# Kernel optimization log

Hardware: AMD Instinct MI355X
Metric: run time of the kernel (lower is better)

Reference implementation:

```python
import jax, jax.numpy as jnp
import numpy as np

NUM_HEADS = 16

def setup_inputs() -> dict:
    key = jax.random.key(0)
    k1, k2, k3 = jax.random.split(key, 3)
    B, S, D = 4, 2048, 1024
    x = jax.random.normal(k1, (B, S, D), dtype=jnp.float32)
    w_qkv = jax.random.normal(k2, (D, 3 * D), dtype=jnp.float32) * (1.0 / np.sqrt(D))
    b_qkv = jnp.zeros((3 * D,), dtype=jnp.float32)
    w_out = jax.random.normal(k3, (D, D), dtype=jnp.float32) * (1.0 / np.sqrt(D))
    b_out = jnp.zeros((D,), dtype=jnp.float32)
    return {"x": x, "w_qkv": w_qkv, "b_qkv": b_qkv, "w_out": w_out, "b_out": b_out}

def reference(x, w_qkv, b_qkv, w_out, b_out):
    B, S, D = x.shape
    H = NUM_HEADS
    Dh = D // H
    # fused QKV projection: [B,S,3D]
    qkv = jnp.einsum('bsd,de->bse', x, w_qkv) + b_qkv
    q, k, v = jnp.split(qkv, 3, axis=-1)
    # separate heads -> [B,H,S,Dh]
    def heads(t):
        return t.reshape(B, S, H, Dh).transpose(0, 2, 1, 3)
    q, k, v = heads(q), heads(k), heads(v)
    # scaled dot-product attention (no mask, no dropout)
    scale = 1.0 / jnp.sqrt(jnp.asarray(Dh, dtype=x.dtype))
    attn = jnp.einsum('bhqd,bhkd->bhqk', q, k) * scale
    weights = jax.nn.softmax(attn, axis=-1)
    out = jnp.einsum('bhqk,bhkd->bhqd', weights, v)
    # combine heads -> [B,S,D], then output projection
    out = out.transpose(0, 2, 1, 3).reshape(B, S, D)
    return jnp.einsum('bsd,de->bse', out, w_out) + b_out
```

## Files before the change

### kernel.cpp

```cpp
#include <hip/hip_runtime.h>

typedef unsigned short u16;
typedef __attribute__((ext_vector_type(8))) short v8s;
typedef __attribute__((ext_vector_type(4))) float v4f;

#define MFMA16(a, b, c) __builtin_amdgcn_mfma_f32_16x16x32_bf16(a, b, c, 0, 0, 0)

static __device__ __forceinline__ u16 f32_to_bf16(float f) {
    unsigned int u = __builtin_bit_cast(unsigned int, f);
    u += 0x7fffu + ((u >> 16) & 1u);
    return (u16)(u >> 16);
}
static __device__ __forceinline__ v8s cvt8(v4f lo, v4f hi) {
    v8s r;
#pragma unroll
    for (int i = 0; i < 4; i++) {
        r[i]     = (short)f32_to_bf16(lo[i]);
        r[i + 4] = (short)f32_to_bf16(hi[i]);
    }
    return r;
}
static __device__ __forceinline__ void gload16(const void* g, void* l) {
    __builtin_amdgcn_global_load_lds(
        (const __attribute__((address_space(1))) unsigned int*)g,
        (__attribute__((address_space(3))) unsigned int*)l, 16, 0, 0);
}

__global__ void transpose_f32_bf16(const float* __restrict__ in,
                                   u16* __restrict__ out, int R, int C) {
    __shared__ u16 t[32][33];
    const int tid = threadIdx.x;
    const int tx = tid & 31, ty = tid >> 5;
    const int c0 = blockIdx.x * 32, r0 = blockIdx.y * 32;
#pragma unroll
    for (int i = 0; i < 32; i += 8)
        t[ty + i][tx] = f32_to_bf16(in[(size_t)(r0 + ty + i) * C + c0 + tx]);
    __syncthreads();
#pragma unroll
    for (int i = 0; i < 32; i += 8)
        out[(size_t)(c0 + ty + i) * R + r0 + tx] = t[tx][ty + i];
}

template <int AMODE, int CMODE>
__global__ __launch_bounds__(256)
void gemm_bt(const void* __restrict__ A, int lda,
             const u16* __restrict__ Bt, int ldb,
             const float* __restrict__ bias,
             void* __restrict__ Cq, u16* __restrict__ Kb, u16* __restrict__ VtG,
             int ldc, int K) {
    constexpr int LDA_T = AMODE ? 48 : 32;
    __shared__ __align__(16) u16 As[128 * LDA_T];
    __shared__ __align__(16) u16 Bs[128 * 32];

    const int tid  = threadIdx.x;
    const int wid  = tid >> 6;
    const int lane = tid & 63;
    const int l15  = lane & 15;
    const int quad = lane >> 4;
    const int bm = blockIdx.y * 128;
    const int bn = blockIdx.x * 128;
    const int wm = (wid & 1) * 64;
    const int wn = (wid >> 1) * 64;

    const int drow = wid * 16 + (lane >> 2);
    const int dcol = (lane & 3) * 8;
    const int ar = tid >> 2;
    const int ag = (tid & 3) * 8;

    const float* Af = (const float*)A;
    const u16*   Au = (const u16*)A;

    v4f acc[4][4];
#pragma unroll
    for (int i = 0; i < 4; i++)
#pragma unroll
        for (int j = 0; j < 4; j++) acc[i][j] = (v4f)0.f;

    for (int kb = 0; kb < K; kb += 32) {
        v8s a0, a1;
        if (AMODE) {
            const float* p0 = Af + (size_t)(bm + ar) * lda + kb + ag;
            const float* p1 = Af + (size_t)(bm + 64 + ar) * lda + kb + ag;
            v4f x00 = *(const v4f*)p0, x01 = *(const v4f*)(p0 + 4);
            v4f x10 = *(const v4f*)p1, x11 = *(const v4f*)(p1 + 4);
            a0 = cvt8(x00, x01);
            a1 = cvt8(x10, x11);
        }
        __syncthreads();
        if (AMODE) {
            *(v8s*)&As[ar * 48 + ag]        = a0;
            *(v8s*)&As[(ar + 64) * 48 + ag] = a1;
        } else {
            gload16(Au + (size_t)(bm + drow) * lda + kb + dcol,
                    &As[drow * 32 + dcol]);
            gload16(Au + (size_t)(bm + 64 + drow) * lda + kb + dcol,
                    &As[(drow + 64) * 32 + dcol]);
        }
        gload16(Bt + (size_t)(bn + drow) * ldb + kb + dcol,
                &Bs[drow * 32 + dcol]);
        gload16(Bt + (size_t)(bn + 64 + drow) * ldb + kb + dcol,
                &Bs[(drow + 64) * 32 + dcol]);
        __syncthreads();

        v8s af[4], bf[4];
#pragma unroll
        for (int mt = 0; mt < 4; mt++)
            af[mt] = *(const v8s*)&As[(wm + mt * 16 + l15) * LDA_T + quad * 8];
#pragma unroll
        for (int nt = 0; nt < 4; nt++)
            bf[nt] = *(const v8s*)&Bs[(wn + nt * 16 + l15) * 32 + quad * 8];
#pragma unroll
        for (int mt = 0; mt < 4; mt++)
#pragma unroll
            for (int nt = 0; nt < 4; nt++)
                acc[mt][nt] = MFMA16(af[mt], bf[nt], acc[mt][nt]);
    }

#pragma unroll
    for (int nt = 0; nt < 4; nt++) {
        const int n = bn + wn + nt * 16 + l15;
        const float bv = bias[n];
#pragma unroll
        for (int mt = 0; mt < 4; mt++) {
#pragma unroll
            for (int r = 0; r < 4; r++) {
                const int m = bm + wm + mt * 16 + quad * 4 + r;
                const float val = acc[mt][nt][r] + bv;
                if (CMODE == 1) {
                    ((float*)Cq)[(size_t)m * ldc + n] = val;
                } else {
                    const u16 o = f32_to_bf16(val);
                    const int region = n >> 10, nl = n & 1023;
                    if (region == 0) {
                        ((u16*)Cq)[(size_t)m * 1024 + nl] = o;
                    } else if (region == 1) {
                        Kb[(size_t)m * 1024 + nl] = o;
                    } else {
                        const int h = nl >> 6, dh = nl & 63;
                        const int b = m >> 11, s = m & 2047;
                        VtG[((size_t)((b * 16 + h) * 64 + dh)) * 2048 + s] = o;
                    }
                }
            }
        }
    }
}

__global__ __launch_bounds__(256)
void attn_fused(u16* __restrict__ Qb, const u16* __restrict__ Kb,
                const u16* __restrict__ VtG) {
    __shared__ __align__(16) u16 Ks[64 * 72];
    __shared__ __align__(16) u16 Vs[64 * 72];
    __shared__ __align__(16) u16 Ps[4 * 16 * 72];

    const int tid  = threadIdx.x;
    const int wid  = tid >> 6;
    const int lane = tid & 63;
    const int l15  = lane & 15;
    const int quad = lane >> 4;
    const int qt = blockIdx.x;
    const int h  = blockIdx.y;
    const int bz = blockIdx.z;

    const size_t qbase = (size_t)bz * 2048 * 1024;
    const int q0 = qt * 64 + wid * 16;
    const u16* qrow = Qb + qbase + (size_t)(q0 + l15) * 1024 + h * 64 + quad * 8;
    const v8s aq0 = *(const v8s*)qrow;
    const v8s aq1 = *(const v8s*)(qrow + 32);

    u16* psw = &Ps[wid * 16 * 72];
    float lrow[4] = {0.f, 0.f, 0.f, 0.f};
    v4f accO[4];
#pragma unroll
    for (int c = 0; c < 4; c++) accO[c] = (v4f)0.f;

    const int sr = tid >> 3;
    const int sg = (tid & 7) * 8;
    const float scale = 0.125f;

    const u16* kpb = Kb + qbase + h * 64;
    const u16* vpb = VtG + (size_t)((bz * 16 + h) * 64) * 2048;

    for (int kt = 0; kt < 32; kt++) {
        const v8s k0 = *(const v8s*)(kpb + (size_t)(kt * 64 + sr) * 1024 + sg);
        const v8s k1 = *(const v8s*)(kpb + (size_t)(kt * 64 + sr + 32) * 1024 + sg);
        const v8s v0 = *(const v8s*)(vpb + (size_t)sr * 2048 + kt * 64 + sg);
        const v8s v1 = *(const v8s*)(vpb + (size_t)(sr + 32) * 2048 + kt * 64 + sg);
        __syncthreads();
        *(v8s*)&Ks[sr * 72 + sg]        = k0;
        *(v8s*)&Ks[(sr + 32) * 72 + sg] = k1;
        *(v8s*)&Vs[sr * 72 + sg]        = v0;
        *(v8s*)&Vs[(sr + 32) * 72 + sg] = v1;
        __syncthreads();

        v4f s[4];
#pragma unroll
        for (int kc = 0; kc < 4; kc++) {
            const v8s kf0 = *(const v8s*)&Ks[(kc * 16 + l15) * 72 + quad * 8];
            const v8s kf1 = *(const v8s*)&Ks[(kc * 16 + l15) * 72 + 32 + quad * 8];
            v4f c = (v4f)0.f;
            c = MFMA16(aq0, kf0, c);
            c = MFMA16(aq1, kf1, c);
            s[kc] = c;
        }

#pragma unroll
        for (int r = 0; r < 4; r++) {
            float rs = 0.f;
#pragma unroll
            for (int kc = 0; kc < 4; kc++) {
                const float p = __expf(s[kc][r] * scale);
                rs += p;
                psw[(quad * 4 + r) * 72 + kc * 16 + l15] = f32_to_bf16(p);
            }
            lrow[r] += rs;
        }
        __threadfence_block();

        const v8s ap0 = *(const v8s*)&psw[l15 * 72 + quad * 8];
        const v8s ap1 = *(const v8s*)&psw[l15 * 72 + 32 + quad * 8];
#pragma unroll
        for (int c = 0; c < 4; c++) {
            const v8s bv0 = *(const v8s*)&Vs[(c * 16 + l15) * 72 + quad * 8];
            const v8s bv1 = *(const v8s*)&Vs[(c * 16 + l15) * 72 + 32 + quad * 8];
            accO[c] = MFMA16(ap0, bv0, accO[c]);
            accO[c] = MFMA16(ap1, bv1, accO[c]);
        }
    }

#pragma unroll
    for (int r = 0; r < 4; r++)
#pragma unroll
        for (int m = 1; m < 16; m <<= 1) lrow[r] += __shfl_xor(lrow[r], m);

#pragma unroll
    for (int c = 0; c < 4; c++) {
#pragma unroll
        for (int r = 0; r < 4; r++) {
            const int q = q0 + quad * 4 + r;
            Qb[qbase + (size_t)q * 1024 + h * 64 + c * 16 + l15] =
                f32_to_bf16(accO[c][r] / lrow[r]);
        }
    }
}

extern "C" void kernel_launch(void* const* d_in, const int* in_sizes, int n_in,
                              void* d_out, int out_size, void* d_ws, size_t ws_size,
                              hipStream_t stream) {
    (void)in_sizes; (void)n_in; (void)out_size;
    const float* x    = (const float*)d_in[0];
    const float* wqkv = (const float*)d_in[1];
    const float* bqkv = (const float*)d_in[2];
    const float* wout = (const float*)d_in[3];
    const float* bout = (const float*)d_in[4];
    float* outp = (float*)d_out;

    char* ws = (char*)d_ws;
    const size_t BIG = 58720256;

    if (ws_size == 0 || ws_size >= BIG) {
        u16* Qb    = (u16*)(ws);
        u16* Kb    = (u16*)(ws + 16777216);
        u16* VtG   = (u16*)(ws + 33554432);
        u16* wqkvT = (u16*)(ws + 50331648);
        u16* woutT = (u16*)(ws + 56623104);

        transpose_f32_bf16<<<dim3(96, 32), 256, 0, stream>>>(wqkv, wqkvT, 1024, 3072);
        transpose_f32_bf16<<<dim3(32, 32), 256, 0, stream>>>(wout, woutT, 1024, 1024);
        gemm_bt<1, 2><<<dim3(24, 64), 256, 0, stream>>>(
            x, 1024, wqkvT, 1024, bqkv, Qb, Kb, VtG, 0, 1024);
        attn_fused<<<dim3(32, 16, 4), 256, 0, stream>>>(Qb, Kb, VtG);
        gemm_bt<0, 1><<<dim3(8, 64), 256, 0, stream>>>(
            Qb, 1024, woutT, 1024, bout, outp, nullptr, nullptr, 1024, 1024);
    } else {
        u16* wqkvT = (u16*)(ws);
        u16* woutT = (u16*)(ws + 6291456);
        u16* Qb    = (u16*)(ws + 8388608);
        u16* Kb    = (u16*)(ws + 12582912);
        u16* VtG   = (u16*)(ws + 16777216);

        transpose_f32_bf16<<<dim3(96, 32), 256, 0, stream>>>(wqkv, wqkvT, 1024, 3072);
        transpose_f32_bf16<<<dim3(32, 32), 256, 0, stream>>>(wout, woutT, 1024, 1024);
        for (int b = 0; b < 4; b++) {
            const float* xb = x + (size_t)b * 2048 * 1024;
            float* ob = outp + (size_t)b * 2048 * 1024;
            gemm_bt<1, 2><<<dim3(24, 16), 256, 0, stream>>>(
                xb, 1024, wqkvT, 1024, bqkv, Qb, Kb, VtG, 0, 1024);
            attn_fused<<<dim3(32, 16, 1), 256, 0, stream>>>(Qb, Kb, VtG);
            gemm_bt<0, 1><<<dim3(8, 16), 256, 0, stream>>>(
                Qb, 1024, woutT, 1024, bout, ob, nullptr, nullptr, 1024, 1024);
        }
    }
}
```

Baseline: 373.0 us.

## Widen GEMM K-tile, pre-cast x to bf16, streamline attention softmax writes

The GEMM now stages 64-wide K slices through registers into padded LDS tiles instead of using direct global-to-LDS loads, which halves the number of barriers per K. When the workspace is large enough, x is cast to bf16 in a separate kernel so the QKV GEMM reads bf16 instead of converting f32 on the fly. The attention kernel computes S transposed so each lane writes a packed 4-element P chunk. It also uses exp2 with a folded scale and reduces the row sum with fewer shuffles. The costs are higher LDS use, an extra kernel launch, and a dependence on workspace size.

Measured after the change: 363.7 us. 1.03x faster.

```diff
diff --git a/kernel.cpp b/kernel.cpp
--- a/kernel.cpp
+++ b/kernel.cpp
@@ -2,6 +2,7 @@
 
 typedef unsigned short u16;
 typedef __attribute__((ext_vector_type(8))) short v8s;
+typedef __attribute__((ext_vector_type(4))) short v4s;
 typedef __attribute__((ext_vector_type(4))) float v4f;
 
 #define MFMA16(a, b, c) __builtin_amdgcn_mfma_f32_16x16x32_bf16(a, b, c, 0, 0, 0)
@@ -20,10 +21,15 @@
     }
     return r;
 }
-static __device__ __forceinline__ void gload16(const void* g, void* l) {
-    __builtin_amdgcn_global_load_lds(
-        (const __attribute__((address_space(1))) unsigned int*)g,
-        (__attribute__((address_space(3))) unsigned int*)l, 16, 0, 0);
+
+__global__ void cast_f32_bf16(const float* __restrict__ in,
+                              u16* __restrict__ out, int n8) {
+    const int i = blockIdx.x * blockDim.x + threadIdx.x;
+    if (i < n8) {
+        v4f lo = ((const v4f*)in)[2 * i];
+        v4f hi = ((const v4f*)in)[2 * i + 1];
+        ((v8s*)out)[i] = cvt8(lo, hi);
+    }
 }
 
 __global__ void transpose_f32_bf16(const float* __restrict__ in,
@@ -48,9 +54,8 @@
              const float* __restrict__ bias,
              void* __restrict__ Cq, u16* __restrict__ Kb, u16* __restrict__ VtG,
              int ldc, int K) {
-    constexpr int LDA_T = AMODE ? 48 : 32;
-    __shared__ __align__(16) u16 As[128 * LDA_T];
-    __shared__ __align__(16) u16 Bs[128 * 32];
+    __shared__ __align__(16) u16 As[128 * 72];
+    __shared__ __align__(16) u16 Bs[128 * 72];
 
     const int tid  = threadIdx.x;
     const int wid  = tid >> 6;
@@ -62,10 +67,8 @@
     const int wm = (wid & 1) * 64;
     const int wn = (wid >> 1) * 64;
 
-    const int drow = wid * 16 + (lane >> 2);
-    const int dcol = (lane & 3) * 8;
-    const int ar = tid >> 2;
-    const int ag = (tid & 3) * 8;
+    const int sr = tid >> 3;
+    const int sg = (tid & 7) * 8;
 
     const float* Af = (const float*)A;
     const u16*   Au = (const u16*)A;
@@ -76,44 +79,45 @@
 #pragma unroll
         for (int j = 0; j < 4; j++) acc[i][j] = (v4f)0.f;
 
-    for (int kb = 0; kb < K; kb += 32) {
-        v8s a0, a1;
-        if (AMODE) {
-            const float* p0 = Af + (size_t)(bm + ar) * lda + kb + ag;
-            const float* p1 = Af + (size_t)(bm + 64 + ar) * lda + kb + ag;
-            v4f x00 = *(const v4f*)p0, x01 = *(const v4f*)(p0 + 4);
-            v4f x10 = *(const v4f*)p1, x11 = *(const v4f*)(p1 + 4);
-            a0 = cvt8(x00, x01);
-            a1 = cvt8(x10, x11);
+    for (int kb = 0; kb < K; kb += 64) {
+        v8s a[4], b[4];
+#pragma unroll
+        for (int i = 0; i < 4; i++) {
+            const int row = sr + i * 32;
+            if (AMODE) {
+                const float* p = Af + (size_t)(bm + row) * lda + kb + sg;
+                a[i] = cvt8(*(const v4f*)p, *(const v4f*)(p + 4));
+            } else {
+                a[i] = *(const v8s*)(Au + (size_t)(bm + row) * lda + kb + sg);
+            }
+            b[i] = *(const v8s*)(Bt + (size_t)(bn + row) * ldb + kb + sg);
         }
         __syncthreads();
-        if (AMODE) {
-            *(v8s*)&As[ar * 48 + ag]        = a0;
-            *(v8s*)&As[(ar + 64) * 48 + ag] = a1;
-        } else {
-            gload16(Au + (size_t)(bm + drow) * lda + kb + dcol,
-                    &As[drow * 32 + dcol]);
-            gload16(Au + (size_t)(bm + 64 + drow) * lda + kb + dcol,
-                    &As[(drow + 64) * 32 + dcol]);
-        }
-        gload16(Bt + (size_t)(bn + drow) * ldb + kb + dcol,
-                &Bs[drow * 32 + dcol]);
-        gload16(Bt + (size_t)(bn + 64 + drow) * ldb + kb + dcol,
-                &Bs[(drow + 64) * 32 + dcol]);
+#pragma unroll
+        for (int i = 0; i < 4; i++) {
+            const int row = sr + i * 32;
+            *(v8s*)&As[row * 72 + sg] = a[i];
+            *(v8s*)&Bs[row * 72 + sg] = b[i];
+        }
         __syncthreads();
 
-        v8s af[4], bf[4];
-#pragma unroll
-        for (int mt = 0; mt < 4; mt++)
-            af[mt] = *(const v8s*)&As[(wm + mt * 16 + l15) * LDA_T + quad * 8];
-#pragma unroll
-        for (int nt = 0; nt < 4; nt++)
-            bf[nt] = *(const v8s*)&Bs[(wn + nt * 16 + l15) * 32 + quad * 8];
-#pragma unroll
-        for (int mt = 0; mt < 4; mt++)
+        v8s af[2][4], bf[2][4];
+#pragma unroll
+        for (int ko = 0; ko < 2; ko++) {
+#pragma unroll
+            for (int mt = 0; mt < 4; mt++)
+                af[ko][mt] = *(const v8s*)&As[(wm + mt * 16 + l15) * 72 + ko * 32 + quad * 8];
 #pragma unroll
             for (int nt = 0; nt < 4; nt++)
-                acc[mt][nt] = MFMA16(af[mt], bf[nt], acc[mt][nt]);
+                bf[ko][nt] = *(const v8s*)&Bs[(wn + nt * 16 + l15) * 72 + ko * 32 + quad * 8];
+        }
+#pragma unroll
+        for (int ko = 0; ko < 2; ko++)
+#pragma unroll
+            for (int mt = 0; mt < 4; mt++)
+#pragma unroll
+                for (int nt = 0; nt < 4; nt++)
+                    acc[mt][nt] = MFMA16(af[ko][mt], bf[ko][nt], acc[mt][nt]);
     }
 
 #pragma unroll
@@ -169,14 +173,14 @@
     const v8s aq1 = *(const v8s*)(qrow + 32);
 
     u16* psw = &Ps[wid * 16 * 72];
-    float lrow[4] = {0.f, 0.f, 0.f, 0.f};
+    float lrow = 0.f;
     v4f accO[4];
 #pragma unroll
     for (int c = 0; c < 4; c++) accO[c] = (v4f)0.f;
 
     const int sr = tid >> 3;
     const int sg = (tid & 7) * 8;
-    const float scale = 0.125f;
+    const float SC = 0.18033688f;
 
     const u16* kpb = Kb + qbase + h * 64;
     const u16* vpb = VtG + (size_t)((bz * 16 + h) * 64) * 2048;
@@ -193,27 +197,23 @@
         *(v8s*)&Vs[(sr + 32) * 72 + sg] = v1;
         __syncthreads();
 
-        v4f s[4];
 #pragma unroll
         for (int kc = 0; kc < 4; kc++) {
             const v8s kf0 = *(const v8s*)&Ks[(kc * 16 + l15) * 72 + quad * 8];
             const v8s kf1 = *(const v8s*)&Ks[(kc * 16 + l15) * 72 + 32 + quad * 8];
-            v4f c = (v4f)0.f;
-            c = MFMA16(aq0, kf0, c);
-            c = MFMA16(aq1, kf1, c);
-            s[kc] = c;
-        }
-
-#pragma unroll
-        for (int r = 0; r < 4; r++) {
+            v4f st = (v4f)0.f;
+            st = MFMA16(kf0, aq0, st);
+            st = MFMA16(kf1, aq1, st);
+            v4s pk;
             float rs = 0.f;
 #pragma unroll
-            for (int kc = 0; kc < 4; kc++) {
-                const float p = __expf(s[kc][r] * scale);
+            for (int r = 0; r < 4; r++) {
+                const float p = exp2f(st[r] * SC);
                 rs += p;
-                psw[(quad * 4 + r) * 72 + kc * 16 + l15] = f32_to_bf16(p);
+                pk[r] = (short)f32_to_bf16(p);
             }
-            lrow[r] += rs;
+            lrow += rs;
+            *(v4s*)&psw[l15 * 72 + kc * 16 + quad * 4] = pk;
         }
         __threadfence_block();
 
@@ -228,10 +228,11 @@
         }
     }
 
-#pragma unroll
-    for (int r = 0; r < 4; r++)
-#pragma unroll
-        for (int m = 1; m < 16; m <<= 1) lrow[r] += __shfl_xor(lrow[r], m);
+    lrow += __shfl_xor(lrow, 16);
+    lrow += __shfl_xor(lrow, 32);
+    float lq[4];
+#pragma unroll
+    for (int r = 0; r < 4; r++) lq[r] = __shfl(lrow, quad * 4 + r);
 
 #pragma unroll
     for (int c = 0; c < 4; c++) {
@@ -239,7 +240,7 @@
         for (int r = 0; r < 4; r++) {
             const int q = q0 + quad * 4 + r;
             Qb[qbase + (size_t)q * 1024 + h * 64 + c * 16 + l15] =
-                f32_to_bf16(accO[c][r] / lrow[r]);
+                f32_to_bf16(accO[c][r] / lq[r]);
         }
     }
 }
@@ -256,19 +257,27 @@
     float* outp = (float*)d_out;
 
     char* ws = (char*)d_ws;
-    const size_t BIG = 58720256;
-
-    if (ws_size == 0 || ws_size >= BIG) {
+    const size_t BIG  = 58720256;
+    const size_t BIGX = 75497472;
+
+    if (ws_size >= BIG || ws_size == 0) {
         u16* Qb    = (u16*)(ws);
         u16* Kb    = (u16*)(ws + 16777216);
         u16* VtG   = (u16*)(ws + 33554432);
         u16* wqkvT = (u16*)(ws + 50331648);
         u16* woutT = (u16*)(ws + 56623104);
+        u16* xb    = (u16*)(ws + 58720256);
 
         transpose_f32_bf16<<<dim3(96, 32), 256, 0, stream>>>(wqkv, wqkvT, 1024, 3072);
         transpose_f32_bf16<<<dim3(32, 32), 256, 0, stream>>>(wout, woutT, 1024, 1024);
-        gemm_bt<1, 2><<<dim3(24, 64), 256, 0, stream>>>(
-            x, 1024, wqkvT, 1024, bqkv, Qb, Kb, VtG, 0, 1024);
+        if (ws_size >= BIGX) {
+            cast_f32_bf16<<<4096, 256, 0, stream>>>(x, xb, 1048576);
+            gemm_bt<0, 2><<<dim3(24, 64), 256, 0, stream>>>(
+                xb, 1024, wqkvT, 1024, bqkv, Qb, Kb, VtG, 0, 1024);
+        } else {
+            gemm_bt<1, 2><<<dim3(24, 64), 256, 0, stream>>>(
+                x, 1024, wqkvT, 1024, bqkv, Qb, Kb, VtG, 0, 1024);
+        }
         attn_fused<<<dim3(32, 16, 4), 256, 0, stream>>>(Qb, Kb, VtG);
         gemm_bt<0, 1><<<dim3(8, 64), 256, 0, stream>>>(
             Qb, 1024, woutT, 1024, bout, outp, nullptr, nullptr, 1024, 1024);
```
